# Performance work log

Measured on AMD Instinct MI355X. Metric: run time of the kernel, lower is better.

## Reference

```python
import jax, jax.numpy as jnp
import numpy as np

N_NODES = 50000
N_GRAPHS = 64


def gcn_layer(x, W, b, src, dst, norm, n):
    # PyG GCNConv: h = x @ W; aggregate norm-weighted messages at dst; add bias
    h = x @ W
    msg = h[src] * norm[:, None]          # [E_tot, out_dim] gather
    out = jax.ops.segment_sum(msg, dst, num_segments=n)
    return out + b


def to_dense_batch(x, batch, max_num, num_graphs):
    n = x.shape[0]
    counts = jax.ops.segment_sum(jnp.ones((n,), x.dtype), batch, num_segments=num_graphs)
    starts = jnp.concatenate([jnp.zeros((1,), jnp.int32),
                              jnp.cumsum(counts.astype(jnp.int32))[:-1]])
    pos = jnp.arange(n, dtype=jnp.int32) - starts[batch]
    valid = pos < max_num
    b_idx = jnp.where(valid, batch, num_graphs)   # overflow -> dummy row
    p_idx = jnp.where(valid, pos, 0)
    dense = jnp.zeros((num_graphs + 1, max_num, x.shape[1]), x.dtype)
    dense = dense.at[b_idx, p_idx].set(x)
    return dense[:num_graphs]


def setup_inputs() -> dict:
    key = jax.random.key(0)
    ks = jax.random.split(key, 12)
    F0, F2, F3, OUT = 54, 108, 216, 200
    x = jax.random.normal(ks[0], (N_NODES, F0), jnp.float32)
    edge_index = jax.random.randint(ks[1], (2, 800000), 0, N_NODES, jnp.int64)
    batch = jnp.sort(jax.random.randint(ks[2], (N_NODES,), 0, N_GRAPHS, jnp.int64))
    def glorot(k, shp):
        lim = 1.0 / np.sqrt(shp[0])
        return jax.random.uniform(k, shp, jnp.float32, -lim, lim)
    return {
        "x": x, "edge_index": edge_index, "batch": batch, "max_num": 1000,
        "W1": glorot(ks[3], (F0, F0)), "b1": jnp.zeros((F0,), jnp.float32),
        "W2": glorot(ks[4], (F0, F2)), "b2": jnp.zeros((F2,), jnp.float32),
        "W3": glorot(ks[5], (F2, F3)), "b3": jnp.zeros((F3,), jnp.float32),
        "Wf": glorot(ks[6], (F3, OUT)), "bf": glorot(ks[7], (OUT,)),
    }


def reference(x, edge_index, batch, max_num, W1, b1, W2, b2, W3, b3, Wf, bf):
    n = x.shape[0]
    loops = jnp.arange(n, dtype=edge_index.dtype)
    src = jnp.concatenate([edge_index[0], loops])
    dst = jnp.concatenate([edge_index[1], loops])
    # symmetric GCN normalization with self-loops (edge_weight = 1)
    deg = jax.ops.segment_sum(jnp.ones_like(dst, jnp.float32), dst, num_segments=n)
    dinv = jax.lax.rsqrt(deg)  # deg >= 1 due to self-loops
    norm = dinv[src] * dinv[dst]

    h = jax.nn.relu(gcn_layer(x, W1, b1, src, dst, norm, n))
    h = jax.nn.relu(gcn_layer(h, W2, b2, src, dst, norm, n))
    h = jax.nn.relu(gcn_layer(h, W3, b3, src, dst, norm, n))
    h = h @ Wf + bf
    return to_dense_batch(h, batch, max_num, N_GRAPHS)
```

## Files before the change

### kernel.cpp

```cpp
#include <hip/hip_runtime.h>
#include <hip/hip_bf16.h>

#define N_GRAPHS 64

typedef __bf16 bf16x8 __attribute__((ext_vector_type(8)));
typedef float floatx4 __attribute__((ext_vector_type(4)));
typedef unsigned short ushort8v __attribute__((ext_vector_type(8)));

template <bool B> struct BoolC { static constexpr bool value = B; };

__device__ __forceinline__ float b2f(unsigned short u) {
    union { unsigned int i; float f; } v;
    v.i = ((unsigned int)u) << 16;
    return v.f;
}
__device__ __forceinline__ unsigned short f2b(float f) {
    __hip_bfloat16 h = __float2bfloat16(f);
    return *(unsigned short*)&h;
}


__global__ void k_deg(const int* __restrict__ dst, int* __restrict__ deg, int E) {
    int e = blockIdx.x * blockDim.x + threadIdx.x;
    if (e < E) atomicAdd(&deg[dst[e]], 1);
}

__global__ void k_scan_blocks(const int* __restrict__ deg, int* __restrict__ row_start,
                              int* __restrict__ blk_sums, int N) {
    __shared__ int s[256];
    int t = threadIdx.x;
    int i = blockIdx.x * 256 + t;
    int v = (i < N) ? deg[i] : 0;
    s[t] = v;
    __syncthreads();
    for (int off = 1; off < 256; off <<= 1) {
        int x = (t >= off) ? s[t - off] : 0;
        __syncthreads();
        s[t] += x;
        __syncthreads();
    }
    if (i < N) row_start[i] = s[t] - v;
    if (t == 255) blk_sums[blockIdx.x] = s[255];
}

__global__ void k_scan_tot(const int* __restrict__ blk_sums, int nb, int* __restrict__ blk_off) {
    __shared__ int s[256];
    int t = threadIdx.x;
    int v = (t < nb) ? blk_sums[t] : 0;
    s[t] = v;
    __syncthreads();
    for (int off = 1; off < 256; off <<= 1) {
        int x = (t >= off) ? s[t - off] : 0;
        __syncthreads();
        s[t] += x;
        __syncthreads();
    }
    if (t < nb) blk_off[t] = s[t] - v;
}

__global__ void k_scan_add(int* __restrict__ row_start, const int* __restrict__ blk_off,
                           int* __restrict__ cursor, const int* __restrict__ deg,
                           float* __restrict__ dinv, const int* __restrict__ batch,
                           int* __restrict__ gstarts, int N, int E) {
    int i = blockIdx.x * 256 + threadIdx.x;
    if (i < N) {
        int r = row_start[i] + blk_off[blockIdx.x];
        row_start[i] = r;
        cursor[i] = r;
        dinv[i] = 1.0f / sqrtf((float)(deg[i] + 1));
        int b = batch[i];
        int prev = (i == 0) ? -1 : batch[i - 1];
        for (int g = prev + 1; g <= b; ++g) gstarts[g] = i;
        if (i == N - 1)
            for (int g = b + 1; g <= N_GRAPHS; ++g) gstarts[g] = N;
    }
    if (i == 0) row_start[N] = E;
}

__global__ void k_fill(const int* __restrict__ src, const int* __restrict__ dst,
                       int* __restrict__ cursor, int2* __restrict__ col2,
                       const float* __restrict__ dinv, int E) {
    int e = blockIdx.x * blockDim.x + threadIdx.x;
    if (e < E) {
        int s = src[e];
        int p = atomicAdd(&cursor[dst[e]], 1);
        col2[p] = make_int2(s, __float_as_int(dinv[s]));
    }
}

__device__ __forceinline__ void swz_one(const float* __restrict__ W,
                                        unsigned short* __restrict__ Wsw, int i, int K, int Nn,
                                        int KS) {
    int j = i & 7, lane = (i >> 3) & 63;
    int ks = (i >> 9) % KS, nt = i / (512 * KS);
    int n = nt * 16 + (lane & 15);
    int k = ks * 32 + (lane >> 4) * 8 + j;
    float v = (k < K && n < Nn) ? W[(size_t)k * Nn + n] : 0.f;
    Wsw[i] = f2b(v);
}

#define T_W1 (4 * 2 * 512)
#define T_W2 (8 * 2 * 512)
#define T_W3 (14 * 4 * 512)
#define T_WF (13 * 7 * 512)

__global__ void k_prep(const float* __restrict__ W1, const float* __restrict__ W2,
                       const float* __restrict__ W3, const float* __restrict__ Wf,
                       unsigned short* __restrict__ W1s, unsigned short* __restrict__ W2s,
                       unsigned short* __restrict__ W3s, unsigned short* __restrict__ Wfs,
                       const float* __restrict__ x, unsigned short* __restrict__ xb, int Nn) {
    int i = blockIdx.x * 256 + threadIdx.x;
    if (i < T_W1) swz_one(W1, W1s, i, 54, 54, 2);
    else if (i < T_W1 + T_W2) swz_one(W2, W2s, i - T_W1, 54, 108, 2);
    else if (i < T_W1 + T_W2 + T_W3) swz_one(W3, W3s, i - T_W1 - T_W2, 108, 216, 4);
    else if (i < T_W1 + T_W2 + T_W3 + T_WF)
        swz_one(Wf, Wfs, i - T_W1 - T_W2 - T_W3, 216, 200, 7);
    else {
        int ii = i - (T_W1 + T_W2 + T_W3 + T_WF);
        if (ii < Nn * 64) {
            int n = ii >> 6, c = ii & 63;
            xb[ii] = (c < 54) ? f2b(x[(size_t)n * 54 + c]) : (unsigned short)0;
        }
    }
}


template <int P, int AS, int NODES, int NG, int ECAP>
__device__ __forceinline__ void gatherP(const unsigned short* __restrict__ in,
                                        const int* __restrict__ row_start,
                                        const int2* __restrict__ col2,
                                        const float* __restrict__ dinv,
                                        unsigned short* agg_s, int2* ecol_s,
                                        int node0, int N, int t) {
    constexpr int S = P / 8;
    constexpr int G = 32 / S;
    constexpr int RPG = NODES / NG;
    constexpr int NTH = NG * 32;
    int grp = t >> 5, lane5 = t & 31;
    int j = lane5 / S, cl = lane5 % S;
    int nlast = node0 + NODES;
    if (nlast > N) nlast = N;
    int block_rs = row_start[node0];
    int block_re = row_start[nlast];
    int rs_a[RPG], re_a[RPG];
    float dn_a[RPG];
    ushort8v self_a[RPG];
#pragma unroll
    for (int rr = 0; rr < RPG; ++rr) {
        int n = node0 + grp + rr * NG;
        bool valid = n < N;
        rs_a[rr] = valid ? row_start[n] : 0;
        re_a[rr] = valid ? row_start[n + 1] : 0;
        dn_a[rr] = valid ? dinv[n] : 0.f;
        if (valid && j == 0)
            self_a[rr] = *((const ushort8v*)(in + (size_t)n * P) + cl);
    }
    int stage = block_re - block_rs;
    if (stage > ECAP) stage = ECAP;
    for (int i = t; i < stage; i += NTH) ecol_s[i] = col2[block_rs + i];
    __syncthreads();

    auto core = [&](auto staged_c) {
        constexpr bool ST = decltype(staged_c)::value;
#pragma unroll
        for (int rr = 0; rr < RPG; ++rr) {
            int r = grp + rr * NG;
            int n = node0 + r;
            float a[8] = {0.f, 0.f, 0.f, 0.f, 0.f, 0.f, 0.f, 0.f};
            if (n < N) {
                float dn = dn_a[rr];
                if (j == 0) {
#pragma unroll
                    for (int i = 0; i < 8; ++i) a[i] = dn * b2f(self_a[rr][i]);
                }
                int re = re_a[rr];
                int e = rs_a[rr] + j;
                for (; e < re; e += 4 * G) {
                    int e1 = min(e + G, re - 1);
                    int e2 = min(e + 2 * G, re - 1);
                    int e3 = min(e + 3 * G, re - 1);
                    int2 c0, c1, c2, c3;
                    if constexpr (ST) {
                        c0 = ecol_s[e - block_rs];
                        c1 = ecol_s[e1 - block_rs];
                        c2 = ecol_s[e2 - block_rs];
                        c3 = ecol_s[e3 - block_rs];
                    } else {
                        c0 = col2[e];
                        c1 = col2[e1];
                        c2 = col2[e2];
                        c3 = col2[e3];
                    }
                    ushort8v v0 = *((const ushort8v*)(in + (size_t)c0.x * P) + cl);
                    ushort8v v1 = *((const ushort8v*)(in + (size_t)c1.x * P) + cl);
                    ushort8v v2 = *((const ushort8v*)(in + (size_t)c2.x * P) + cl);
                    ushort8v v3 = *((const ushort8v*)(in + (size_t)c3.x * P) + cl);
                    float d0 = __int_as_float(c0.y);
                    float d1 = (e + G < re) ? __int_as_float(c1.y) : 0.f;
                    float d2 = (e + 2 * G < re) ? __int_as_float(c2.y) : 0.f;
                    float d3 = (e + 3 * G < re) ? __int_as_float(c3.y) : 0.f;
#pragma unroll
                    for (int i = 0; i < 8; ++i) {
                        a[i] += d0 * b2f(v0[i]) + d1 * b2f(v1[i]);
                        a[i] += d2 * b2f(v2[i]) + d3 * b2f(v3[i]);
                    }
                }
#pragma unroll
                for (int i = 0; i < 8; ++i) a[i] *= dn;
            }
#pragma unroll
            for (int mask = S; mask < 32; mask <<= 1)
#pragma unroll
                for (int i = 0; i < 8; ++i) a[i] += __shfl_xor(a[i], mask, 32);
            if (j == 0) {
                ushort8v rv;
#pragma unroll
                for (int i = 0; i < 8; ++i) rv[i] = f2b(a[i]);
                *((ushort8v*)(agg_s + r * AS) + cl) = rv;
            }
        }
    };
    if (block_re - block_rs <= ECAP) core(BoolC<true>{});
    else core(BoolC<false>{});
}


template <int P, int FOUT, int FP, int KS, int NT>
__global__ __launch_bounds__(128) void k_layer(
    const unsigned short* __restrict__ in, const int* __restrict__ row_start,
    const int2* __restrict__ col2, const float* __restrict__ dinv,
    const unsigned short* __restrict__ Wsw, const float* __restrict__ bias,
    unsigned short* __restrict__ hout, int N) {
    constexpr int AS = KS * 32 + 8;
    __shared__ __align__(16) unsigned short agg_s[16 * AS];
    __shared__ __align__(16) int2 ecol_s[512];
    int node0 = blockIdx.x * 16;
    int t = threadIdx.x;
    gatherP<P, AS, 16, 4, 512>(in, row_start, col2, dinv, agg_s, ecol_s, node0, N, t);
    __syncthreads();
    int lane = t & 63, wv = t >> 6, m = lane & 15, q = lane >> 4;
    bf16x8 a[KS];
#pragma unroll
    for (int ks = 0; ks < KS; ++ks)
        a[ks] = *(const bf16x8*)(agg_s + m * AS + ks * 32 + q * 8);
    for (int nt = wv; nt < NT; nt += 2) {
        const unsigned short* bp = Wsw + ((size_t)(nt * KS) * 64 + lane) * 8;
        bf16x8 bfr[KS];
#pragma unroll
        for (int ks = 0; ks < KS; ++ks) bfr[ks] = *(const bf16x8*)(bp + ks * 512);
        int fo = nt * 16 + m;
        float bb = (fo < FOUT) ? bias[fo] : 0.f;
        floatx4 c = {0.f, 0.f, 0.f, 0.f};
#pragma unroll
        for (int ks = 0; ks < KS; ++ks)
            c = __builtin_amdgcn_mfma_f32_16x16x32_bf16(a[ks], bfr[ks], c, 0, 0, 0);
#pragma unroll
        for (int r = 0; r < 4; ++r) {
            int n = node0 + q * 4 + r;
            if (n < N) hout[(size_t)n * FP + fo] = f2b(fmaxf(c[r] + bb, 0.f));
        }
    }
}


__global__ __launch_bounds__(256) void k_l3f(
    const unsigned short* __restrict__ h2, const int* __restrict__ row_start,
    const int2* __restrict__ col2, const float* __restrict__ dinv,
    const unsigned short* __restrict__ W3s, const float* __restrict__ b3,
    const unsigned short* __restrict__ Wfs, const float* __restrict__ bfv,
    const int* __restrict__ batch, const int* __restrict__ gstarts, float* __restrict__ out,
    int N, int mn) {
    constexpr int AS = 136, HS = 232;
    __shared__ __align__(16) unsigned short smem[32 * HS];
    __shared__ __align__(16) int2 ecol_s[1024];
    unsigned short* agg_s = smem;
    unsigned short* h3_s = smem;
    int node0 = blockIdx.x * 32;
    int t = threadIdx.x;
    gatherP<128, AS, 32, 8, 1024>(h2, row_start, col2, dinv, agg_s, ecol_s, node0, N, t);
    __syncthreads();
    int lane = t & 63, wv = t >> 6, m = lane & 15, q = lane >> 4;
    bf16x8 a1[2][4];
#pragma unroll
    for (int mt = 0; mt < 2; ++mt)
#pragma unroll
        for (int ks = 0; ks < 4; ++ks)
            a1[mt][ks] = *(const bf16x8*)(agg_s + (mt * 16 + m) * AS + ks * 32 + q * 8);
    __syncthreads();
    for (int nt = wv; nt < 14; nt += 4) {
        const unsigned short* bp = W3s + ((size_t)(nt * 4) * 64 + lane) * 8;
        bf16x8 bf0 = *(const bf16x8*)(bp);
        bf16x8 bf1 = *(const bf16x8*)(bp + 512);
        bf16x8 bf2 = *(const bf16x8*)(bp + 1024);
        bf16x8 bf3 = *(const bf16x8*)(bp + 1536);
        int fo = nt * 16 + m;
        float bb = (fo < 216) ? b3[fo] : 0.f;
#pragma unroll
        for (int mt = 0; mt < 2; ++mt) {
            floatx4 c = {0.f, 0.f, 0.f, 0.f};
            c = __builtin_amdgcn_mfma_f32_16x16x32_bf16(a1[mt][0], bf0, c, 0, 0, 0);
            c = __builtin_amdgcn_mfma_f32_16x16x32_bf16(a1[mt][1], bf1, c, 0, 0, 0);
            c = __builtin_amdgcn_mfma_f32_16x16x32_bf16(a1[mt][2], bf2, c, 0, 0, 0);
            c = __builtin_amdgcn_mfma_f32_16x16x32_bf16(a1[mt][3], bf3, c, 0, 0, 0);
#pragma unroll
            for (int r = 0; r < 4; ++r) {
                int row = mt * 16 + q * 4 + r;
                h3_s[row * HS + fo] = f2b(fmaxf(c[r] + bb, 0.f));
            }
        }
    }
    __syncthreads();
    bf16x8 a2[2][7];
#pragma unroll
    for (int mt = 0; mt < 2; ++mt)
#pragma unroll
        for (int ks = 0; ks < 7; ++ks)
            a2[mt][ks] = *(const bf16x8*)(h3_s + (mt * 16 + m) * HS + ks * 32 + q * 8);
    for (int nt = wv; nt < 13; nt += 4) {
        const unsigned short* bp = Wfs + ((size_t)(nt * 7) * 64 + lane) * 8;
        bf16x8 bfr[7];
#pragma unroll
        for (int ks = 0; ks < 7; ++ks) bfr[ks] = *(const bf16x8*)(bp + ks * 512);
        int fo = nt * 16 + m;
        if (fo >= 200) continue;
        float bb = bfv[fo];
#pragma unroll
        for (int mt = 0; mt < 2; ++mt) {
            floatx4 c = {0.f, 0.f, 0.f, 0.f};
#pragma unroll
            for (int ks = 0; ks < 7; ++ks)
                c = __builtin_amdgcn_mfma_f32_16x16x32_bf16(a2[mt][ks], bfr[ks], c, 0, 0, 0);
#pragma unroll
            for (int r = 0; r < 4; ++r) {
                int n = node0 + mt * 16 + q * 4 + r;
                if (n < N) {
                    int b = batch[n];
                    int pos = n - gstarts[b];
                    if (pos >= 0 && pos < mn)
                        out[((size_t)b * mn + pos) * 200 + fo] = c[r] + bb;
                }
            }
        }
    }
}

extern "C" void kernel_launch(void* const* d_in, const int* in_sizes, int n_in,
                              void* d_out, int out_size, void* d_ws, size_t ws_size,
                              hipStream_t stream) {
    const float* x = (const float*)d_in[0];
    const int* ei = (const int*)d_in[1];
    const int* batch = (const int*)d_in[2];
    const float* W1 = (const float*)d_in[4];
    const float* b1 = (const float*)d_in[5];
    const float* W2 = (const float*)d_in[6];
    const float* b2 = (const float*)d_in[7];
    const float* W3 = (const float*)d_in[8];
    const float* b3 = (const float*)d_in[9];
    const float* Wf = (const float*)d_in[10];
    const float* bfv = (const float*)d_in[11];
    float* out = (float*)d_out;

    const int N = in_sizes[2];
    const int E = in_sizes[1] / 2;
    const int mn = out_size / (N_GRAPHS * 200);
    const int* src = ei;
    const int* dst = ei + E;

    char* w = (char*)d_ws;
    auto alloc = [&](size_t bytes) {
        void* p = (void*)w;
        w += (bytes + 255) & ~(size_t)255;
        return p;
    };
    int* deg = (int*)alloc((size_t)N * 4);
    int* row_start = (int*)alloc((size_t)(N + 1) * 4);
    int* blk_sums = (int*)alloc(256 * 4);
    int* blk_off = (int*)alloc(256 * 4);
    int* cursor = (int*)alloc((size_t)N * 4);
    int2* col2 = (int2*)alloc((size_t)E * 8);
    float* dinv = (float*)alloc((size_t)N * 4);
    int* gstarts = (int*)alloc((N_GRAPHS + 1) * 4);
    unsigned short* xb = (unsigned short*)alloc((size_t)N * 64 * 2);
    unsigned short* h1 = (unsigned short*)alloc((size_t)N * 64 * 2);
    unsigned short* h2 = (unsigned short*)alloc((size_t)N * 128 * 2);
    unsigned short* W1s = (unsigned short*)alloc((size_t)T_W1 * 2);
    unsigned short* W2s = (unsigned short*)alloc((size_t)T_W2 * 2);
    unsigned short* W3s = (unsigned short*)alloc((size_t)T_W3 * 2);
    unsigned short* Wfs = (unsigned short*)alloc((size_t)T_WF * 2);
    (void)ws_size;

    hipMemsetAsync(deg, 0, (size_t)N * 4, stream);
    hipMemsetAsync(d_out, 0, (size_t)out_size * sizeof(float), stream);

    int NB = (N + 255) / 256;
    k_deg<<<(E + 255) / 256, 256, 0, stream>>>(dst, deg, E);
    k_scan_blocks<<<NB, 256, 0, stream>>>(deg, row_start, blk_sums, N);
    k_scan_tot<<<1, 256, 0, stream>>>(blk_sums, NB, blk_off);
    k_scan_add<<<NB, 256, 0, stream>>>(row_start, blk_off, cursor, deg, dinv, batch, gstarts,
                                       N, E);
    k_fill<<<(E + 255) / 256, 256, 0, stream>>>(src, dst, cursor, col2, dinv, E);
    int prep_total = T_W1 + T_W2 + T_W3 + T_WF + N * 64;
    k_prep<<<(prep_total + 255) / 256, 256, 0, stream>>>(W1, W2, W3, Wf, W1s, W2s, W3s, Wfs,
                                                         x, xb, N);

    int NBL16 = (N + 15) / 16;
    k_layer<64, 54, 64, 2, 4><<<NBL16, 128, 0, stream>>>(xb, row_start, col2, dinv, W1s, b1,
                                                         h1, N);
    k_layer<64, 108, 128, 2, 8><<<NBL16, 128, 0, stream>>>(h1, row_start, col2, dinv, W2s,
                                                           b2, h2, N);
    int NBL32 = (N + 31) / 32;
    k_l3f<<<NBL32, 256, 0, stream>>>(h2, row_start, col2, dinv, W3s, b3, Wfs, bfv, batch,
                                     gstarts, out, N, mn);
}
```

Before: 323.1 us.

## Interleave gathers of two nodes per group and drop LDS edge staging

The gather now processes two destination rows at once in an interleaved loop, issuing eight independent row loads per iteration to raise memory-level parallelism. It removes the shared-memory staging of edge column/weight pairs and its extra block barrier, reading col2 straight from global memory instead. This frees LDS and one sync per block but adds register pressure and tail loops for the unequal-length rows.

```diff
diff --git a/kernel.cpp b/kernel.cpp
--- a/kernel.cpp
+++ b/kernel.cpp
@@ -6,8 +6,6 @@
 typedef __bf16 bf16x8 __attribute__((ext_vector_type(8)));
 typedef float floatx4 __attribute__((ext_vector_type(4)));
 typedef unsigned short ushort8v __attribute__((ext_vector_type(8)));
-
-template <bool B> struct BoolC { static constexpr bool value = B; };
 
 __device__ __forceinline__ float b2f(unsigned short u) {
     union { unsigned int i; float f; } v;
@@ -125,26 +123,19 @@
 }
 
 
-template <int P, int AS, int NODES, int NG, int ECAP>
+template <int P, int AS, int NODES, int NG>
 __device__ __forceinline__ void gatherP(const unsigned short* __restrict__ in,
                                         const int* __restrict__ row_start,
                                         const int2* __restrict__ col2,
                                         const float* __restrict__ dinv,
-                                        unsigned short* agg_s, int2* ecol_s,
-                                        int node0, int N, int t) {
+                                        unsigned short* agg_s, int node0, int N, int t) {
     constexpr int S = P / 8;
     constexpr int G = 32 / S;
     constexpr int RPG = NODES / NG;
-    constexpr int NTH = NG * 32;
     int grp = t >> 5, lane5 = t & 31;
     int j = lane5 / S, cl = lane5 % S;
-    int nlast = node0 + NODES;
-    if (nlast > N) nlast = N;
-    int block_rs = row_start[node0];
-    int block_re = row_start[nlast];
     int rs_a[RPG], re_a[RPG];
     float dn_a[RPG];
-    ushort8v self_a[RPG];
 #pragma unroll
     for (int rr = 0; rr < RPG; ++rr) {
         int n = node0 + grp + rr * NG;
@@ -152,76 +143,120 @@
         rs_a[rr] = valid ? row_start[n] : 0;
         re_a[rr] = valid ? row_start[n + 1] : 0;
         dn_a[rr] = valid ? dinv[n] : 0.f;
-        if (valid && j == 0)
-            self_a[rr] = *((const ushort8v*)(in + (size_t)n * P) + cl);
-    }
-    int stage = block_re - block_rs;
-    if (stage > ECAP) stage = ECAP;
-    for (int i = t; i < stage; i += NTH) ecol_s[i] = col2[block_rs + i];
-    __syncthreads();
-
-    auto core = [&](auto staged_c) {
-        constexpr bool ST = decltype(staged_c)::value;
-#pragma unroll
-        for (int rr = 0; rr < RPG; ++rr) {
-            int r = grp + rr * NG;
-            int n = node0 + r;
-            float a[8] = {0.f, 0.f, 0.f, 0.f, 0.f, 0.f, 0.f, 0.f};
-            if (n < N) {
-                float dn = dn_a[rr];
-                if (j == 0) {
-#pragma unroll
-                    for (int i = 0; i < 8; ++i) a[i] = dn * b2f(self_a[rr][i]);
-                }
-                int re = re_a[rr];
-                int e = rs_a[rr] + j;
-                for (; e < re; e += 4 * G) {
-                    int e1 = min(e + G, re - 1);
-                    int e2 = min(e + 2 * G, re - 1);
-                    int e3 = min(e + 3 * G, re - 1);
-                    int2 c0, c1, c2, c3;
-                    if constexpr (ST) {
-                        c0 = ecol_s[e - block_rs];
-                        c1 = ecol_s[e1 - block_rs];
-                        c2 = ecol_s[e2 - block_rs];
-                        c3 = ecol_s[e3 - block_rs];
-                    } else {
-                        c0 = col2[e];
-                        c1 = col2[e1];
-                        c2 = col2[e2];
-                        c3 = col2[e3];
-                    }
-                    ushort8v v0 = *((const ushort8v*)(in + (size_t)c0.x * P) + cl);
-                    ushort8v v1 = *((const ushort8v*)(in + (size_t)c1.x * P) + cl);
-                    ushort8v v2 = *((const ushort8v*)(in + (size_t)c2.x * P) + cl);
-                    ushort8v v3 = *((const ushort8v*)(in + (size_t)c3.x * P) + cl);
-                    float d0 = __int_as_float(c0.y);
-                    float d1 = (e + G < re) ? __int_as_float(c1.y) : 0.f;
-                    float d2 = (e + 2 * G < re) ? __int_as_float(c2.y) : 0.f;
-                    float d3 = (e + 3 * G < re) ? __int_as_float(c3.y) : 0.f;
-#pragma unroll
-                    for (int i = 0; i < 8; ++i) {
-                        a[i] += d0 * b2f(v0[i]) + d1 * b2f(v1[i]);
-                        a[i] += d2 * b2f(v2[i]) + d3 * b2f(v3[i]);
-                    }
-                }
-#pragma unroll
-                for (int i = 0; i < 8; ++i) a[i] *= dn;
-            }
-#pragma unroll
-            for (int mask = S; mask < 32; mask <<= 1)
-#pragma unroll
-                for (int i = 0; i < 8; ++i) a[i] += __shfl_xor(a[i], mask, 32);
-            if (j == 0) {
-                ushort8v rv;
-#pragma unroll
-                for (int i = 0; i < 8; ++i) rv[i] = f2b(a[i]);
-                *((ushort8v*)(agg_s + r * AS) + cl) = rv;
-            }
-        }
-    };
-    if (block_re - block_rs <= ECAP) core(BoolC<true>{});
-    else core(BoolC<false>{});
+    }
+#pragma unroll
+    for (int pp = 0; pp < RPG; pp += 2) {
+        int rA = grp + pp * NG, rB = grp + (pp + 1) * NG;
+        int nA = node0 + rA, nB = node0 + rB;
+        float aA[8] = {0.f, 0.f, 0.f, 0.f, 0.f, 0.f, 0.f, 0.f};
+        float aB[8] = {0.f, 0.f, 0.f, 0.f, 0.f, 0.f, 0.f, 0.f};
+        float dnA = dn_a[pp], dnB = dn_a[pp + 1];
+        if (j == 0) {
+            if (nA < N) {
+                ushort8v u = *((const ushort8v*)(in + (size_t)nA * P) + cl);
+#pragma unroll
+                for (int i = 0; i < 8; ++i) aA[i] = dnA * b2f(u[i]);
+            }
+            if (nB < N) {
+                ushort8v u = *((const ushort8v*)(in + (size_t)nB * P) + cl);
+#pragma unroll
+                for (int i = 0; i < 8; ++i) aB[i] = dnB * b2f(u[i]);
+            }
+        }
+        int reA = re_a[pp], reB = re_a[pp + 1];
+        int eA = rs_a[pp] + j, eB = rs_a[pp + 1] + j;
+        while (eA < reA && eB < reB) {
+            int a1 = min(eA + G, reA - 1), a2 = min(eA + 2 * G, reA - 1),
+                a3 = min(eA + 3 * G, reA - 1);
+            int b1 = min(eB + G, reB - 1), b2 = min(eB + 2 * G, reB - 1),
+                b3 = min(eB + 3 * G, reB - 1);
+            int2 cA0 = col2[eA], cA1 = col2[a1], cA2 = col2[a2], cA3 = col2[a3];
+            int2 cB0 = col2[eB], cB1 = col2[b1], cB2 = col2[b2], cB3 = col2[b3];
+            ushort8v vA0 = *((const ushort8v*)(in + (size_t)cA0.x * P) + cl);
+            ushort8v vA1 = *((const ushort8v*)(in + (size_t)cA1.x * P) + cl);
+            ushort8v vA2 = *((const ushort8v*)(in + (size_t)cA2.x * P) + cl);
+            ushort8v vA3 = *((const ushort8v*)(in + (size_t)cA3.x * P) + cl);
+            ushort8v vB0 = *((const ushort8v*)(in + (size_t)cB0.x * P) + cl);
+            ushort8v vB1 = *((const ushort8v*)(in + (size_t)cB1.x * P) + cl);
+            ushort8v vB2 = *((const ushort8v*)(in + (size_t)cB2.x * P) + cl);
+            ushort8v vB3 = *((const ushort8v*)(in + (size_t)cB3.x * P) + cl);
+            float dA0 = __int_as_float(cA0.y);
+            float dA1 = (eA + G < reA) ? __int_as_float(cA1.y) : 0.f;
+            float dA2 = (eA + 2 * G < reA) ? __int_as_float(cA2.y) : 0.f;
+            float dA3 = (eA + 3 * G < reA) ? __int_as_float(cA3.y) : 0.f;
+            float dB0 = __int_as_float(cB0.y);
+            float dB1 = (eB + G < reB) ? __int_as_float(cB1.y) : 0.f;
+            float dB2 = (eB + 2 * G < reB) ? __int_as_float(cB2.y) : 0.f;
+            float dB3 = (eB + 3 * G < reB) ? __int_as_float(cB3.y) : 0.f;
+#pragma unroll
+            for (int i = 0; i < 8; ++i) {
+                aA[i] += dA0 * b2f(vA0[i]) + dA1 * b2f(vA1[i]);
+                aA[i] += dA2 * b2f(vA2[i]) + dA3 * b2f(vA3[i]);
+                aB[i] += dB0 * b2f(vB0[i]) + dB1 * b2f(vB1[i]);
+                aB[i] += dB2 * b2f(vB2[i]) + dB3 * b2f(vB3[i]);
+            }
+            eA += 4 * G;
+            eB += 4 * G;
+        }
+        for (; eA < reA; eA += 4 * G) {
+            int a1 = min(eA + G, reA - 1), a2 = min(eA + 2 * G, reA - 1),
+                a3 = min(eA + 3 * G, reA - 1);
+            int2 c0 = col2[eA], c1 = col2[a1], c2 = col2[a2], c3 = col2[a3];
+            ushort8v v0 = *((const ushort8v*)(in + (size_t)c0.x * P) + cl);
+            ushort8v v1 = *((const ushort8v*)(in + (size_t)c1.x * P) + cl);
+            ushort8v v2 = *((const ushort8v*)(in + (size_t)c2.x * P) + cl);
+            ushort8v v3 = *((const ushort8v*)(in + (size_t)c3.x * P) + cl);
+            float d0 = __int_as_float(c0.y);
+            float d1 = (eA + G < reA) ? __int_as_float(c1.y) : 0.f;
+            float d2 = (eA + 2 * G < reA) ? __int_as_float(c2.y) : 0.f;
+            float d3 = (eA + 3 * G < reA) ? __int_as_float(c3.y) : 0.f;
+#pragma unroll
+            for (int i = 0; i < 8; ++i) {
+                aA[i] += d0 * b2f(v0[i]) + d1 * b2f(v1[i]);
+                aA[i] += d2 * b2f(v2[i]) + d3 * b2f(v3[i]);
+            }
+        }
+        for (; eB < reB; eB += 4 * G) {
+            int b1 = min(eB + G, reB - 1), b2 = min(eB + 2 * G, reB - 1),
+                b3 = min(eB + 3 * G, reB - 1);
+            int2 c0 = col2[eB], c1 = col2[b1], c2 = col2[b2], c3 = col2[b3];
+            ushort8v v0 = *((const ushort8v*)(in + (size_t)c0.x * P) + cl);
+            ushort8v v1 = *((const ushort8v*)(in + (size_t)c1.x * P) + cl);
+            ushort8v v2 = *((const ushort8v*)(in + (size_t)c2.x * P) + cl);
+            ushort8v v3 = *((const ushort8v*)(in + (size_t)c3.x * P) + cl);
+            float d0 = __int_as_float(c0.y);
+            float d1 = (eB + G < reB) ? __int_as_float(c1.y) : 0.f;
+            float d2 = (eB + 2 * G < reB) ? __int_as_float(c2.y) : 0.f;
+            float d3 = (eB + 3 * G < reB) ? __int_as_float(c3.y) : 0.f;
+#pragma unroll
+            for (int i = 0; i < 8; ++i) {
+                aB[i] += d0 * b2f(v0[i]) + d1 * b2f(v1[i]);
+                aB[i] += d2 * b2f(v2[i]) + d3 * b2f(v3[i]);
+            }
+        }
+#pragma unroll
+        for (int i = 0; i < 8; ++i) {
+            aA[i] *= dnA;
+            aB[i] *= dnB;
+        }
+#pragma unroll
+        for (int mask = S; mask < 32; mask <<= 1)
+#pragma unroll
+            for (int i = 0; i < 8; ++i) {
+                aA[i] += __shfl_xor(aA[i], mask, 32);
+                aB[i] += __shfl_xor(aB[i], mask, 32);
+            }
+        if (j == 0) {
+            ushort8v rvA, rvB;
+#pragma unroll
+            for (int i = 0; i < 8; ++i) {
+                rvA[i] = f2b(aA[i]);
+                rvB[i] = f2b(aB[i]);
+            }
+            *((ushort8v*)(agg_s + rA * AS) + cl) = rvA;
+            *((ushort8v*)(agg_s + rB * AS) + cl) = rvB;
+        }
+    }
 }
 
 
@@ -233,10 +268,9 @@
     unsigned short* __restrict__ hout, int N) {
     constexpr int AS = KS * 32 + 8;
     __shared__ __align__(16) unsigned short agg_s[16 * AS];
-    __shared__ __align__(16) int2 ecol_s[512];
     int node0 = blockIdx.x * 16;
     int t = threadIdx.x;
-    gatherP<P, AS, 16, 4, 512>(in, row_start, col2, dinv, agg_s, ecol_s, node0, N, t);
+    gatherP<P, AS, 16, 4>(in, row_start, col2, dinv, agg_s, node0, N, t);
     __syncthreads();
     int lane = t & 63, wv = t >> 6, m = lane & 15, q = lane >> 4;
     bf16x8 a[KS];
@@ -272,12 +306,11 @@
     int N, int mn) {
     constexpr int AS = 136, HS = 232;
     __shared__ __align__(16) unsigned short smem[32 * HS];
-    __shared__ __align__(16) int2 ecol_s[1024];
     unsigned short* agg_s = smem;
     unsigned short* h3_s = smem;
     int node0 = blockIdx.x * 32;
     int t = threadIdx.x;
-    gatherP<128, AS, 32, 8, 1024>(h2, row_start, col2, dinv, agg_s, ecol_s, node0, N, t);
+    gatherP<128, AS, 32, 8>(h2, row_start, col2, dinv, agg_s, node0, N, t);
     __syncthreads();
     int lane = t & 63, wv = t >> 6, m = lane & 15, q = lane >> 4;
     bf16x8 a1[2][4];
```

Result: no change. 326.4 us (+1.0%).
